# Kernel optimization log

Hardware: AMD Instinct MI355X
Metric: run time of the kernel (lower is better)

## Reference

```python
import jax, jax.numpy as jnp
import numpy as np

# Static problem sizes (must be static for segment ops under jit)
N = 2048   # num nodes (seq_len)
M = 50     # num hyperedges (hyper_num); original uses max(edge_id)+1, guaranteed hit with 8192 draws
C = 64     # out_channels (= in_channels here)
BT = 64    # batch
E = 8192   # incidences = k(=4) hyperedges per node
NEG_SLOPE = 0.2
MARGIN = 4.2


def setup_inputs() -> dict:
    key = jax.random.key(0)
    k1, k2, k3, k4, k5 = jax.random.split(key, 5)
    x = jax.random.normal(k1, (BT, N, C), jnp.float32)
    weight = jax.random.normal(k2, (C, C), jnp.float32) * (1.0 / np.sqrt(C))  # glorot-ish
    att = jax.random.normal(k3, (1, 1, 2 * C), jnp.float32) * 0.1
    node_idx = jax.random.randint(k4, (E,), 0, N, dtype=jnp.int32)
    edge_idx = jax.random.randint(k5, (E,), 0, M, dtype=jnp.int32)
    return {"x": x, "weight": weight, "att": att, "node_idx": node_idx, "edge_idx": edge_idx}


def _safe_norm(v, axis):
    # norm with zero (not NaN/inf) gradient at 0, matching torch.norm subgradient
    sq = jnp.sum(v * v, axis=axis)
    pos = sq > 0
    return jnp.where(pos, jnp.sqrt(jnp.where(pos, sq, 1.0)), 0.0)


def _segment_softmax(logits, seg, num_segments):
    # grouped softmax over incidences sharing the same node id (PyG softmax)
    mx = jax.ops.segment_max(logits, seg, num_segments=num_segments)
    mx = jnp.where(jnp.isfinite(mx), mx, 0.0)  # empty segments
    e = jnp.exp(logits - mx[seg])
    s = jax.ops.segment_sum(e, seg, num_segments=num_segments)
    return e / (s[seg] + 1e-16)


def reference(x, weight, att, node_idx, edge_idx):
    xw = jnp.einsum('bnc,cd->bnd', x, weight)          # [B,N,C] dense GEMM
    x1 = jnp.transpose(xw, (1, 0, 2))                  # [N,B,C]
    x_i = x1[node_idx]                                 # [E,B,C] gather per incidence
    edge_sums = jax.ops.segment_sum(x_i, edge_idx, num_segments=M)  # [M,B,C] per-edge aggregate
    x_j = edge_sums[edge_idx]                          # [E,B,C]

    # pairwise hyperedge contrastive loss (vectorized double loop over edges)
    inner = jnp.einsum('kbc,mbc->kmb', edge_sums, edge_sums)  # [M,M,B]
    nrm = _safe_norm(edge_sums, axis=-1)               # [M,B]
    cos = inner / (nrm[:, None, :] * nrm[None, :, :])
    diff = edge_sums[:, None] - edge_sums[None, :]     # [M,M,B,C]
    dist = _safe_norm(diff, axis=-1)                   # [M,M,B]
    loss_item = cos * dist + (1.0 - cos) * jnp.maximum(MARGIN - dist, 0.0)
    loss_hyper = jnp.sum(jnp.abs(jnp.mean(loss_item, axis=-1))) / float((M + 1) ** 2)

    # per-incidence attention, softmax grouped by node
    logits = jnp.sum(jnp.concatenate([x_i, x_j], axis=-1) * att.reshape(1, 1, 2 * C), axis=-1)  # [E,B]
    logits = jax.nn.leaky_relu(logits, NEG_SLOPE)
    alpha = _segment_softmax(logits, node_idx, N)      # [E,B] (dropout skipped: eval mode)

    ones = jnp.ones((E,), xw.dtype)
    D = jax.ops.segment_sum(ones, node_idx, num_segments=N)    # node degree
    Bdeg = jax.ops.segment_sum(ones, edge_idx, num_segments=M) # hyperedge degree
    Bnorm = jnp.where(Bdeg > 0, 1.0 / Bdeg, 0.0)

    # propagate pass 1: nodes -> hyperedges (source_to_target)
    msg1 = Bnorm[edge_idx][:, None, None] * alpha[:, :, None] * x_i
    edge_feat = jax.ops.segment_sum(msg1, edge_idx, num_segments=M)  # [M,B,C]
    # propagate pass 2: hyperedges -> nodes (target_to_source)
    msg2 = D[node_idx][:, None, None] * alpha[:, :, None] * edge_feat[edge_idx]
    out = jax.ops.segment_sum(msg2, node_idx, num_segments=N)        # [N,B,C]
    out = jnp.transpose(out, (1, 0, 2))               # [B,N,C]

    constrain_losstotal = jnp.abs(jnp.mean(x_i - x_j)) + loss_hyper
    return out, constrain_losstotal
```

## Files before the change

kernel.cpp:

```cpp
#include <hip/hip_runtime.h>
#include <math.h>

#define NN 2048
#define MM 50
#define CC 64
#define BB 64
#define EE 8192
#define NEG 0.2f
#define MARGIN_ 4.2f
#define ETILE 320
#define NPAIRBLK 625

__global__ __launch_bounds__(256) void k_build(const int* __restrict__ nidx,const int* __restrict__ eidx,
                        int* __restrict__ ncnt,int* __restrict__ noff,
                        int* __restrict__ ecnt,int* __restrict__ eoff,
                        int* __restrict__ nlist,int* __restrict__ elist){
  int t=threadIdx.x, wv=t>>6, lane=t&63;
  int seg = blockIdx.x*4 + wv;
  if (seg >= NN+MM) return;
  const int* key; int target; int* outl;
  if (seg < NN){ key=nidx; target=seg;    outl=nlist; }
  else         { key=eidx; target=seg-NN; outl=elist; }
  int base = 0;
  for (int e=lane; e<EE; e+=64) base += (key[e] < target);
  #pragma unroll
  for (int m=32;m>=1;m>>=1) base += __shfl_xor(base,m,64);
  unsigned long long ltmask = (1ull<<lane) - 1ull;
  int carry = 0;
  for (int wq=0; wq<EE/64; ++wq){
    int e = wq*64 + lane;
    bool mm = (key[e]==target);
    unsigned long long bal = __ballot(mm);
    if (mm) outl[base + carry + __popcll(bal & ltmask)] = e;
    carry += __popcll(bal);
  }
  if (lane==0){
    if (seg<NN){ ncnt[seg]=carry; noff[seg]=base; }
    else       { ecnt[seg-NN]=carry; eoff[seg-NN]=base; }
  }
}

__global__ __launch_bounds__(256) void k_gemm(const float* __restrict__ x,const float* __restrict__ w,
       const float* __restrict__ att, float* __restrict__ outf,
       float* __restrict__ natt1,float* __restrict__ natt2,
       const int* __restrict__ ncnt, float* __restrict__ gpart2){
  __shared__ float Xl[64*68];
  __shared__ float Wl[64*64];
  __shared__ float red[16];
  int t = threadIdx.x;
  size_t rbase = (size_t)blockIdx.x*64;
  {
    const float4* xs = (const float4*)(x + rbase*CC);
    const float4* wsrc = (const float4*)w;
    #pragma unroll
    for (int i=0;i<4;++i){
      int idx = t + i*256;
      int r = idx>>4, c4 = idx&15;
      float4 v = xs[idx];
      *(float4*)&Xl[r*68 + c4*4] = v;
      ((float4*)Wl)[idx] = wsrc[idx];
    }
  }
  __syncthreads();
  int rg = t>>4, cg = t&15;
  int c0 = cg*4;
  float acc[4][4];
  #pragma unroll
  for (int i=0;i<4;++i){ acc[i][0]=0.f; acc[i][1]=0.f; acc[i][2]=0.f; acc[i][3]=0.f; }
  #pragma unroll
  for (int ks=0; ks<16; ++ks){
    int k0 = ks*4;
    float4 Wf0 = *(const float4*)&Wl[(k0+0)*64 + c0];
    float4 Wf1 = *(const float4*)&Wl[(k0+1)*64 + c0];
    float4 Wf2 = *(const float4*)&Wl[(k0+2)*64 + c0];
    float4 Wf3 = *(const float4*)&Wl[(k0+3)*64 + c0];
    #pragma unroll
    for (int ri=0;ri<4;++ri){
      float4 Xf = *(const float4*)&Xl[(rg*4+ri)*68 + k0];
      acc[ri][0] += Xf.x*Wf0.x; acc[ri][1] += Xf.x*Wf0.y; acc[ri][2] += Xf.x*Wf0.z; acc[ri][3] += Xf.x*Wf0.w;
      acc[ri][0] += Xf.y*Wf1.x; acc[ri][1] += Xf.y*Wf1.y; acc[ri][2] += Xf.y*Wf1.z; acc[ri][3] += Xf.y*Wf1.w;
      acc[ri][0] += Xf.z*Wf2.x; acc[ri][1] += Xf.z*Wf2.y; acc[ri][2] += Xf.z*Wf2.z; acc[ri][3] += Xf.z*Wf2.w;
      acc[ri][0] += Xf.w*Wf3.x; acc[ri][1] += Xf.w*Wf3.y; acc[ri][2] += Xf.w*Wf3.z; acc[ri][3] += Xf.w*Wf3.w;
    }
  }
  #pragma unroll
  for (int ri=0;ri<4;++ri){
    size_t row = rbase + rg*4 + ri;
    *(float4*)&outf[row*CC + c0] = make_float4(acc[ri][0],acc[ri][1],acc[ri][2],acc[ri][3]);
  }
  float4 at1 = *(const float4*)(att + c0);
  float4 at2 = *(const float4*)(att + CC + c0);
  float prs = 0.f;
  #pragma unroll
  for (int ri=0;ri<4;++ri){
    float a1 = acc[ri][0]*at1.x + acc[ri][1]*at1.y + acc[ri][2]*at1.z + acc[ri][3]*at1.w;
    float a2 = acc[ri][0]*at2.x + acc[ri][1]*at2.y + acc[ri][2]*at2.z + acc[ri][3]*at2.w;
    float rs = (acc[ri][0]+acc[ri][1]) + (acc[ri][2]+acc[ri][3]);
    #pragma unroll
    for (int m=8;m>=1;m>>=1){
      a1 += __shfl_xor(a1,m,64);
      a2 += __shfl_xor(a2,m,64);
      rs += __shfl_xor(rs,m,64);
    }
    if (cg==0){
      size_t row = rbase + rg*4 + ri;
      int b = (int)(row>>11), n = (int)(row&(NN-1));
      natt1[n*BB+b]=a1; natt2[n*BB+b]=a2;
      prs += rs*(float)ncnt[n];
    }
  }
  if (cg==0) red[rg] = prs;
  __syncthreads();
  if (t==0){
    float s=0.f;
    #pragma unroll
    for (int i=0;i<16;++i) s += red[i];
    gpart2[blockIdx.x] = s;
  }
}

__global__ __launch_bounds__(256) void k_eatt(const int* __restrict__ elist,const int* __restrict__ eoff,
                       const int* __restrict__ ecnt,const int* __restrict__ nidx,
                       const float* __restrict__ natt2,float* __restrict__ eatt2){
  __shared__ int lds_n[ETILE];
  __shared__ float part[256];
  int m=blockIdx.x, t=threadIdx.x;
  int b = t&63, ck = t>>6;
  int off=eoff[m], deg=ecnt[m];
  float s=0.f;
  for (int tb=0; tb<deg; tb+=ETILE){
    int tl = min(ETILE, deg-tb);
    __syncthreads();
    for (int j=t;j<tl;j+=256) lds_n[j]=nidx[elist[off+tb+j]];
    __syncthreads();
    int j0=(tl*ck)>>2, j1=(tl*(ck+1))>>2;
    for (int j=j0;j<j1;++j) s += natt2[lds_n[j]*BB+b];
  }
  part[t]=s; __syncthreads();
  if (t<64) eatt2[m*BB+b] = (part[b]+part[64+b])+(part[128+b]+part[192+b]);
}

__global__ void k_alpha(const int* __restrict__ nlist,const int* __restrict__ noff,
                        const int* __restrict__ ncnt,const int* __restrict__ eidx,
                        const float* __restrict__ natt1,const float* __restrict__ eatt2,
                        float* __restrict__ alpha){
  int n = blockIdx.x, b = threadIdx.x;
  int off = noff[n], deg = ncnt[n];
  if (deg==0) return;
  float na = natt1[n*BB+b];
  float mx = -1e30f;
  for (int j=0;j<deg;++j){
    int e = nlist[off+j]; int m = eidx[e];
    float l = na + eatt2[m*BB+b]; l = l>0.f? l : NEG*l;
    mx = fmaxf(mx,l);
  }
  float s=0.f;
  for (int j=0;j<deg;++j){
    int e = nlist[off+j]; int m = eidx[e];
    float l = na + eatt2[m*BB+b]; l = l>0.f? l : NEG*l;
    s += expf(l-mx);
  }
  float inv = 1.f/(s+1e-16f);
  for (int j=0;j<deg;++j){
    int e = nlist[off+j]; int m = eidx[e];
    float l = na + eatt2[m*BB+b]; l = l>0.f? l : NEG*l;
    alpha[(size_t)e*BB+b] = expf(l-mx)*inv;
  }
}

__global__ __launch_bounds__(256) void k_edge(const int* __restrict__ elist,const int* __restrict__ eoff,
                       const int* __restrict__ ecnt,const int* __restrict__ nidx,
                       const float* __restrict__ outf,const float* __restrict__ alpha,
                       float* __restrict__ es,float* __restrict__ ef,float* __restrict__ nrm,
                       float* __restrict__ gpart3){
  __shared__ int   lds_e[ETILE];
  __shared__ int   lds_n[ETILE];
  __shared__ float lds_al[ETILE*16];
  __shared__ float red2[256];
  int m = blockIdx.x>>2, bq = blockIdx.x&3;
  int t = threadIdx.x;
  int bi = t>>4;
  int b  = bq*16 + bi;
  int c0 = (t&15)*4;
  int off = eoff[m], deg = ecnt[m];
  float4 as=make_float4(0.f,0.f,0.f,0.f), af=as;
  for (int tb=0; tb<deg; tb+=ETILE){
    int tl = min(ETILE, deg-tb);
    __syncthreads();
    for (int j=t;j<tl;j+=256){
      int e = elist[off+tb+j];
      lds_e[j]=e; lds_n[j]=nidx[e];
    }
    __syncthreads();
    for (int idx=t; idx<tl*16; idx+=256){
      int j=idx>>4, b2=idx&15;
      lds_al[idx] = alpha[(size_t)lds_e[j]*BB + bq*16 + b2];
    }
    __syncthreads();
    #pragma unroll 4
    for (int j=0;j<tl;++j){
      int n = lds_n[j];
      float al = lds_al[j*16+bi];
      float4 v = *(const float4*)&outf[(size_t)b*(NN*CC) + (size_t)n*CC + c0];
      as.x+=v.x; as.y+=v.y; as.z+=v.z; as.w+=v.w;
      af.x+=al*v.x; af.y+=al*v.y; af.z+=al*v.z; af.w+=al*v.w;
    }
  }
  float bn = deg>0 ? 1.f/(float)deg : 0.f;
  size_t o = ((size_t)m*BB+b)*CC+c0;
  *(float4*)&es[o]=as;
  float4 f; f.x=af.x*bn; f.y=af.y*bn; f.z=af.z*bn; f.w=af.w*bn;
  *(float4*)&ef[o]=f;
  float ssq = as.x*as.x+as.y*as.y+as.z*as.z+as.w*as.w;
  #pragma unroll
  for (int s=8;s>=1;s>>=1) ssq += __shfl_xor(ssq,s,64);
  if ((t&15)==0) nrm[m*BB+b] = ssq>0.f? sqrtf(ssq):0.f;
  red2[t] = (as.x+as.y)+(as.z+as.w);
  __syncthreads();
  for (int s=128;s>0;s>>=1){ if(t<s) red2[t]+=red2[t+s]; __syncthreads(); }
  if (t==0) gpart3[blockIdx.x] = red2[0]*(float)deg;
}

__global__ __launch_bounds__(256) void k_pairout(const float* __restrict__ es,const float* __restrict__ nrm,
                      float* __restrict__ pairl,
                      const int* __restrict__ nlist,const int* __restrict__ noff,
                      const int* __restrict__ ncnt,const int* __restrict__ eidx,
                      const float* __restrict__ alpha,const float* __restrict__ ef,
                      float* __restrict__ outf){
  int bid = blockIdx.x;
  int t = threadIdx.x;
  if (bid < NPAIRBLK){
    int wv = t>>6, b = t&63;
    int km = bid*4 + wv;
    if (km < MM*MM){
      int kk = km / MM, m = km % MM;
      const float4* pa = (const float4*)&es[((size_t)kk*BB+b)*CC];
      const float4* pb = (const float4*)&es[((size_t)m*BB+b)*CC];
      float inner=0.f, d2=0.f;
      #pragma unroll
      for (int q=0;q<16;++q){
        float4 a=pa[q], c=pb[q];
        inner += a.x*c.x+a.y*c.y+a.z*c.z+a.w*c.w;
        float dx=a.x-c.x, dy=a.y-c.y, dz=a.z-c.z, dw=a.w-c.w;
        d2 += dx*dx+dy*dy+dz*dz+dw*dw;
      }
      float dist = d2>0.f? sqrtf(d2):0.f;
      float cosv = inner/(nrm[kk*BB+b]*nrm[m*BB+b]);
      float li = cosv*dist + (1.f-cosv)*fmaxf(MARGIN_-dist,0.f);
      #pragma unroll
      for (int s=32;s>=1;s>>=1) li += __shfl_xor(li,s,64);
      if (b==0) pairl[km] = fabsf(li*(1.f/64.f));
    }
    return;
  }
  int n = bid - NPAIRBLK;
  int b = t>>2, sub = t&3;
  int off = noff[n], deg = ncnt[n];
  float4 a0=make_float4(0.f,0.f,0.f,0.f),a1=a0,a2=a0,a3=a0;
  for (int j=0;j<deg;++j){
    int e = nlist[off+j]; int m = eidx[e];
    float al = alpha[(size_t)e*BB+b];
    const float4* p = (const float4*)&ef[((size_t)m*BB+b)*CC + sub*16];
    float4 v0=p[0],v1=p[1],v2=p[2],v3=p[3];
    a0.x+=al*v0.x; a0.y+=al*v0.y; a0.z+=al*v0.z; a0.w+=al*v0.w;
    a1.x+=al*v1.x; a1.y+=al*v1.y; a1.z+=al*v1.z; a1.w+=al*v1.w;
    a2.x+=al*v2.x; a2.y+=al*v2.y; a2.z+=al*v2.z; a2.w+=al*v2.w;
    a3.x+=al*v3.x; a3.y+=al*v3.y; a3.z+=al*v3.z; a3.w+=al*v3.w;
  }
  float D=(float)deg;
  float* o = &outf[(size_t)b*(NN*CC) + (size_t)n*CC + sub*16];
  ((float4*)o)[0]=make_float4(D*a0.x,D*a0.y,D*a0.z,D*a0.w);
  ((float4*)o)[1]=make_float4(D*a1.x,D*a1.y,D*a1.z,D*a1.w);
  ((float4*)o)[2]=make_float4(D*a2.x,D*a2.y,D*a2.z,D*a2.w);
  ((float4*)o)[3]=make_float4(D*a3.x,D*a3.y,D*a3.z,D*a3.w);
}

__global__ void k_lfin(const float* __restrict__ pairl,const float* __restrict__ gpart2,
                       const float* __restrict__ gpart3, float* __restrict__ out){
  __shared__ float r1[256],r2[256],r3[256];
  int t=threadIdx.x;
  float s1=0.f,s2=0.f,s3=0.f;
  for (int i=t;i<MM*MM;i+=256) s1+=pairl[i];
  for (int i=t;i<(NN*BB)/64;i+=256) s2+=gpart2[i];
  for (int i=t;i<MM*4;i+=256) s3+=gpart3[i];
  r1[t]=s1;r2[t]=s2;r3[t]=s3; __syncthreads();
  for (int s=128;s>0;s>>=1){ if(t<s){r1[t]+=r1[t+s];r2[t]+=r2[t+s];r3[t]+=r3[t+s];} __syncthreads(); }
  if (t==0){
    float lh = r1[0]/2601.f;
    float con = fabsf((r2[0]-r3[0])*(1.f/33554432.f));
    out[(size_t)NN*BB*CC] = con+lh;
  }
}

extern "C" void kernel_launch(void* const* d_in, const int* in_sizes, int n_in,
                              void* d_out, int out_size, void* d_ws, size_t ws_size,
                              hipStream_t stream){
  (void)in_sizes; (void)n_in; (void)out_size; (void)ws_size;
  const float* x    = (const float*)d_in[0];
  const float* w    = (const float*)d_in[1];
  const float* att  = (const float*)d_in[2];
  const int*   nidx = (const int*)d_in[3];
  const int*   eidx = (const int*)d_in[4];
  float* outf = (float*)d_out;

  char* ws = (char*)d_ws;
  size_t off = 0;
  auto alloc = [&](size_t bytes)->void*{ void* p = ws + off; off = (off + bytes + 255) & ~(size_t)255; return p; };
  float* natt1 = (float*)alloc(sizeof(float)*NN*BB);
  float* natt2 = (float*)alloc(sizeof(float)*NN*BB);
  float* eatt2 = (float*)alloc(sizeof(float)*MM*BB);
  float* alpha = (float*)alloc(sizeof(float)*(size_t)EE*BB);
  float* es    = (float*)alloc(sizeof(float)*MM*BB*CC);
  float* ef    = (float*)alloc(sizeof(float)*MM*BB*CC);
  float* nrm   = (float*)alloc(sizeof(float)*MM*BB);
  float* pairl = (float*)alloc(sizeof(float)*MM*MM);
  float* gpart2= (float*)alloc(sizeof(float)*(NN*BB)/64);
  float* gpart3= (float*)alloc(sizeof(float)*MM*4);
  int* ncnt = (int*)alloc(sizeof(int)*NN);
  int* noff = (int*)alloc(sizeof(int)*NN);
  int* ecnt = (int*)alloc(sizeof(int)*MM);
  int* eoff = (int*)alloc(sizeof(int)*MM);
  int* nlist= (int*)alloc(sizeof(int)*EE);
  int* elist= (int*)alloc(sizeof(int)*EE);

  k_build  <<<(NN+MM+3)/4, 256, 0, stream>>>(nidx, eidx, ncnt, noff, ecnt, eoff, nlist, elist);
  k_gemm   <<<(NN*BB)/64, 256, 0, stream>>>(x, w, att, outf, natt1, natt2, ncnt, gpart2);
  k_eatt   <<<MM, 256, 0, stream>>>(elist, eoff, ecnt, nidx, natt2, eatt2);
  k_alpha  <<<NN, 64, 0, stream>>>(nlist, noff, ncnt, eidx, natt1, eatt2, alpha);
  k_edge   <<<MM*4, 256, 0, stream>>>(elist, eoff, ecnt, nidx, outf, alpha, es, ef, nrm, gpart3);
  k_pairout<<<NPAIRBLK + NN, 256, 0, stream>>>(es, nrm, pairl, nlist, noff, ncnt, eidx, alpha, ef, outf);
  k_lfin   <<<1, 256, 0, stream>>>(pairl, gpart2, gpart3, outf);
}
```

Baseline: 139.6 us.

## Merge index build with GEMM and reorganize kernel schedule into five launches

Runs the CSR index build and the x·W GEMM as one launch, with the build done by the first block range. The edge-attention term is now computed from the per-edge sums (att2 dotted with the summed features), which drops the natt2 buffer and the separate k_eatt pass. The edge-sum and norm work moves into an earlier kernel that also reduces the degree-weighted row sums. The pairwise loss now shares a launch with the softmax, and the final scalar reduction runs as an extra block of the output kernel. This cuts the launch count from seven to five and removes some scattered gathers. In exchange, the outf feature rows are read twice, once in k_es and again in k_ef, and the rowsum buffer costs an extra write and read.

```diff
diff --git a/kernel.cpp b/kernel.cpp
--- a/kernel.cpp
+++ b/kernel.cpp
@@ -10,45 +10,47 @@
 #define MARGIN_ 4.2f
 #define ETILE 320
 #define NPAIRBLK 625
-
-__global__ __launch_bounds__(256) void k_build(const int* __restrict__ nidx,const int* __restrict__ eidx,
-                        int* __restrict__ ncnt,int* __restrict__ noff,
-                        int* __restrict__ ecnt,int* __restrict__ eoff,
-                        int* __restrict__ nlist,int* __restrict__ elist){
-  int t=threadIdx.x, wv=t>>6, lane=t&63;
-  int seg = blockIdx.x*4 + wv;
-  if (seg >= NN+MM) return;
-  const int* key; int target; int* outl;
-  if (seg < NN){ key=nidx; target=seg;    outl=nlist; }
-  else         { key=eidx; target=seg-NN; outl=elist; }
-  int base = 0;
-  for (int e=lane; e<EE; e+=64) base += (key[e] < target);
-  #pragma unroll
-  for (int m=32;m>=1;m>>=1) base += __shfl_xor(base,m,64);
-  unsigned long long ltmask = (1ull<<lane) - 1ull;
-  int carry = 0;
-  for (int wq=0; wq<EE/64; ++wq){
-    int e = wq*64 + lane;
-    bool mm = (key[e]==target);
-    unsigned long long bal = __ballot(mm);
-    if (mm) outl[base + carry + __popcll(bal & ltmask)] = e;
-    carry += __popcll(bal);
-  }
-  if (lane==0){
-    if (seg<NN){ ncnt[seg]=carry; noff[seg]=base; }
-    else       { ecnt[seg-NN]=carry; eoff[seg-NN]=base; }
-  }
-}
-
-__global__ __launch_bounds__(256) void k_gemm(const float* __restrict__ x,const float* __restrict__ w,
-       const float* __restrict__ att, float* __restrict__ outf,
-       float* __restrict__ natt1,float* __restrict__ natt2,
-       const int* __restrict__ ncnt, float* __restrict__ gpart2){
+#define NBUILD 525
+
+__global__ __launch_bounds__(256) void k_bg(
+    const float* __restrict__ x, const float* __restrict__ w, const float* __restrict__ att,
+    const int* __restrict__ nidx, const int* __restrict__ eidx,
+    float* __restrict__ outf, float* __restrict__ natt1, float* __restrict__ rsBN,
+    int* __restrict__ ncnt, int* __restrict__ noff, int* __restrict__ ecnt,
+    int* __restrict__ eoff, int* __restrict__ nlist, int* __restrict__ elist){
   __shared__ float Xl[64*68];
   __shared__ float Wl[64*64];
-  __shared__ float red[16];
   int t = threadIdx.x;
-  size_t rbase = (size_t)blockIdx.x*64;
+  int bid = blockIdx.x;
+
+  if (bid < NBUILD){
+    int wv=t>>6, lane=t&63;
+    int seg = bid*4 + wv;
+    if (seg >= NN+MM) return;
+    const int* key; int target; int* outl;
+    if (seg < NN){ key=nidx; target=seg;    outl=nlist; }
+    else         { key=eidx; target=seg-NN; outl=elist; }
+    int base = 0;
+    for (int e=lane; e<EE; e+=64) base += (key[e] < target);
+    #pragma unroll
+    for (int m=32;m>=1;m>>=1) base += __shfl_xor(base,m,64);
+    unsigned long long ltmask = (1ull<<lane) - 1ull;
+    int carry = 0;
+    for (int wq=0; wq<EE/64; ++wq){
+      int e = wq*64 + lane;
+      bool mm = (key[e]==target);
+      unsigned long long bal = __ballot(mm);
+      if (mm) outl[base + carry + __popcll(bal & ltmask)] = e;
+      carry += __popcll(bal);
+    }
+    if (lane==0){
+      if (seg<NN){ ncnt[seg]=carry; noff[seg]=base; }
+      else       { ecnt[seg-NN]=carry; eoff[seg-NN]=base; }
+    }
+    return;
+  }
+
+  size_t rbase = (size_t)(bid - NBUILD)*64;
   {
     const float4* xs = (const float4*)(x + rbase*CC);
     const float4* wsrc = (const float4*)w;
@@ -89,62 +91,115 @@
     *(float4*)&outf[row*CC + c0] = make_float4(acc[ri][0],acc[ri][1],acc[ri][2],acc[ri][3]);
   }
   float4 at1 = *(const float4*)(att + c0);
-  float4 at2 = *(const float4*)(att + CC + c0);
-  float prs = 0.f;
   #pragma unroll
   for (int ri=0;ri<4;++ri){
     float a1 = acc[ri][0]*at1.x + acc[ri][1]*at1.y + acc[ri][2]*at1.z + acc[ri][3]*at1.w;
-    float a2 = acc[ri][0]*at2.x + acc[ri][1]*at2.y + acc[ri][2]*at2.z + acc[ri][3]*at2.w;
     float rs = (acc[ri][0]+acc[ri][1]) + (acc[ri][2]+acc[ri][3]);
     #pragma unroll
     for (int m=8;m>=1;m>>=1){
       a1 += __shfl_xor(a1,m,64);
-      a2 += __shfl_xor(a2,m,64);
       rs += __shfl_xor(rs,m,64);
     }
     if (cg==0){
       size_t row = rbase + rg*4 + ri;
       int b = (int)(row>>11), n = (int)(row&(NN-1));
-      natt1[n*BB+b]=a1; natt2[n*BB+b]=a2;
-      prs += rs*(float)ncnt[n];
-    }
-  }
-  if (cg==0) red[rg] = prs;
-  __syncthreads();
-  if (t==0){
-    float s=0.f;
-    #pragma unroll
-    for (int i=0;i<16;++i) s += red[i];
-    gpart2[blockIdx.x] = s;
-  }
-}
-
-__global__ __launch_bounds__(256) void k_eatt(const int* __restrict__ elist,const int* __restrict__ eoff,
-                       const int* __restrict__ ecnt,const int* __restrict__ nidx,
-                       const float* __restrict__ natt2,float* __restrict__ eatt2){
+      natt1[n*BB+b]=a1; rsBN[row]=rs;
+    }
+  }
+}
+
+__global__ __launch_bounds__(256) void k_es(
+    const int* __restrict__ elist,const int* __restrict__ eoff,
+    const int* __restrict__ ecnt,const int* __restrict__ nidx,
+    const float* __restrict__ outf,const float* __restrict__ att,
+    float* __restrict__ es,float* __restrict__ nrm,float* __restrict__ eatt2,
+    float* __restrict__ gpart3,
+    const float* __restrict__ rsBN,const int* __restrict__ ncnt,
+    float* __restrict__ gpart2){
   __shared__ int lds_n[ETILE];
-  __shared__ float part[256];
-  int m=blockIdx.x, t=threadIdx.x;
-  int b = t&63, ck = t>>6;
-  int off=eoff[m], deg=ecnt[m];
-  float s=0.f;
+  __shared__ float red2[256];
+  int bid = blockIdx.x, t = threadIdx.x;
+
+  if (bid >= MM*4){
+    int k = bid - MM*4;
+    float s = 0.f;
+    for (int i=k*256+t; i<NN*BB; i+=32*256) s += rsBN[i]*(float)ncnt[i&(NN-1)];
+    red2[t]=s; __syncthreads();
+    for (int st=128;st>0;st>>=1){ if(t<st) red2[t]+=red2[t+st]; __syncthreads(); }
+    if (t==0) gpart2[k]=red2[0];
+    return;
+  }
+
+  int m = bid>>2, bq = bid&3;
+  int bi = t>>4;
+  int b  = bq*16 + bi;
+  int c0 = (t&15)*4;
+  int off = eoff[m], deg = ecnt[m];
+  float4 as=make_float4(0.f,0.f,0.f,0.f);
   for (int tb=0; tb<deg; tb+=ETILE){
     int tl = min(ETILE, deg-tb);
     __syncthreads();
     for (int j=t;j<tl;j+=256) lds_n[j]=nidx[elist[off+tb+j]];
     __syncthreads();
-    int j0=(tl*ck)>>2, j1=(tl*(ck+1))>>2;
-    for (int j=j0;j<j1;++j) s += natt2[lds_n[j]*BB+b];
-  }
-  part[t]=s; __syncthreads();
-  if (t<64) eatt2[m*BB+b] = (part[b]+part[64+b])+(part[128+b]+part[192+b]);
-}
-
-__global__ void k_alpha(const int* __restrict__ nlist,const int* __restrict__ noff,
-                        const int* __restrict__ ncnt,const int* __restrict__ eidx,
-                        const float* __restrict__ natt1,const float* __restrict__ eatt2,
-                        float* __restrict__ alpha){
-  int n = blockIdx.x, b = threadIdx.x;
+    #pragma unroll 4
+    for (int j=0;j<tl;++j){
+      int n = lds_n[j];
+      float4 v = *(const float4*)&outf[(size_t)b*(NN*CC) + (size_t)n*CC + c0];
+      as.x+=v.x; as.y+=v.y; as.z+=v.z; as.w+=v.w;
+    }
+  }
+  size_t o = ((size_t)m*BB+b)*CC+c0;
+  *(float4*)&es[o]=as;
+  float ssq = as.x*as.x+as.y*as.y+as.z*as.z+as.w*as.w;
+  float4 at2 = *(const float4*)(att + CC + c0);
+  float ea = as.x*at2.x+as.y*at2.y+as.z*at2.z+as.w*at2.w;
+  #pragma unroll
+  for (int s=8;s>=1;s>>=1){ ssq += __shfl_xor(ssq,s,64); ea += __shfl_xor(ea,s,64); }
+  if ((t&15)==0){
+    nrm[m*BB+b] = ssq>0.f? sqrtf(ssq):0.f;
+    eatt2[m*BB+b] = ea;
+  }
+  red2[t] = (as.x+as.y)+(as.z+as.w);
+  __syncthreads();
+  for (int s=128;s>0;s>>=1){ if(t<s) red2[t]+=red2[t+s]; __syncthreads(); }
+  if (t==0) gpart3[bid] = red2[0]*(float)deg;
+}
+
+__global__ __launch_bounds__(256) void k_ap(
+    const float* __restrict__ es,const float* __restrict__ nrm,
+    float* __restrict__ pairl,
+    const int* __restrict__ nlist,const int* __restrict__ noff,
+    const int* __restrict__ ncnt,const int* __restrict__ eidx,
+    const float* __restrict__ natt1,const float* __restrict__ eatt2,
+    float* __restrict__ alpha){
+  int bid = blockIdx.x, t = threadIdx.x;
+  int wv = t>>6, b = t&63;
+
+  if (bid < NPAIRBLK){
+    int km = bid*4 + wv;
+    if (km >= MM*MM) return;
+    int kk = km / MM, m = km % MM;
+    const float4* pa = (const float4*)&es[((size_t)kk*BB+b)*CC];
+    const float4* pb = (const float4*)&es[((size_t)m*BB+b)*CC];
+    float inner=0.f, d2=0.f;
+    #pragma unroll
+    for (int q=0;q<16;++q){
+      float4 a=pa[q], c=pb[q];
+      inner += a.x*c.x+a.y*c.y+a.z*c.z+a.w*c.w;
+      float dx=a.x-c.x, dy=a.y-c.y, dz=a.z-c.z, dw=a.w-c.w;
+      d2 += dx*dx+dy*dy+dz*dz+dw*dw;
+    }
+    float dist = d2>0.f? sqrtf(d2):0.f;
+    float cosv = inner/(nrm[kk*BB+b]*nrm[m*BB+b]);
+    float li = cosv*dist + (1.f-cosv)*fmaxf(MARGIN_-dist,0.f);
+    #pragma unroll
+    for (int s=32;s>=1;s>>=1) li += __shfl_xor(li,s,64);
+    if (b==0) pairl[km] = fabsf(li*(1.f/64.f));
+    return;
+  }
+
+  int n = (bid - NPAIRBLK)*4 + wv;
+  if (n >= NN) return;
   int off = noff[n], deg = ncnt[n];
   if (deg==0) return;
   float na = natt1[n*BB+b];
@@ -168,22 +223,21 @@
   }
 }
 
-__global__ __launch_bounds__(256) void k_edge(const int* __restrict__ elist,const int* __restrict__ eoff,
-                       const int* __restrict__ ecnt,const int* __restrict__ nidx,
-                       const float* __restrict__ outf,const float* __restrict__ alpha,
-                       float* __restrict__ es,float* __restrict__ ef,float* __restrict__ nrm,
-                       float* __restrict__ gpart3){
+__global__ __launch_bounds__(256) void k_ef(
+    const int* __restrict__ elist,const int* __restrict__ eoff,
+    const int* __restrict__ ecnt,const int* __restrict__ nidx,
+    const float* __restrict__ outf,const float* __restrict__ alpha,
+    float* __restrict__ ef){
   __shared__ int   lds_e[ETILE];
   __shared__ int   lds_n[ETILE];
   __shared__ float lds_al[ETILE*16];
-  __shared__ float red2[256];
   int m = blockIdx.x>>2, bq = blockIdx.x&3;
   int t = threadIdx.x;
   int bi = t>>4;
   int b  = bq*16 + bi;
   int c0 = (t&15)*4;
   int off = eoff[m], deg = ecnt[m];
-  float4 as=make_float4(0.f,0.f,0.f,0.f), af=as;
+  float4 af=make_float4(0.f,0.f,0.f,0.f);
   for (int tb=0; tb<deg; tb+=ETILE){
     int tl = min(ETILE, deg-tb);
     __syncthreads();
@@ -202,58 +256,41 @@
       int n = lds_n[j];
       float al = lds_al[j*16+bi];
       float4 v = *(const float4*)&outf[(size_t)b*(NN*CC) + (size_t)n*CC + c0];
-      as.x+=v.x; as.y+=v.y; as.z+=v.z; as.w+=v.w;
       af.x+=al*v.x; af.y+=al*v.y; af.z+=al*v.z; af.w+=al*v.w;
     }
   }
   float bn = deg>0 ? 1.f/(float)deg : 0.f;
   size_t o = ((size_t)m*BB+b)*CC+c0;
-  *(float4*)&es[o]=as;
   float4 f; f.x=af.x*bn; f.y=af.y*bn; f.z=af.z*bn; f.w=af.w*bn;
   *(float4*)&ef[o]=f;
-  float ssq = as.x*as.x+as.y*as.y+as.z*as.z+as.w*as.w;
-  #pragma unroll
-  for (int s=8;s>=1;s>>=1) ssq += __shfl_xor(ssq,s,64);
-  if ((t&15)==0) nrm[m*BB+b] = ssq>0.f? sqrtf(ssq):0.f;
-  red2[t] = (as.x+as.y)+(as.z+as.w);
-  __syncthreads();
-  for (int s=128;s>0;s>>=1){ if(t<s) red2[t]+=red2[t+s]; __syncthreads(); }
-  if (t==0) gpart3[blockIdx.x] = red2[0]*(float)deg;
-}
-
-__global__ __launch_bounds__(256) void k_pairout(const float* __restrict__ es,const float* __restrict__ nrm,
-                      float* __restrict__ pairl,
-                      const int* __restrict__ nlist,const int* __restrict__ noff,
-                      const int* __restrict__ ncnt,const int* __restrict__ eidx,
-                      const float* __restrict__ alpha,const float* __restrict__ ef,
-                      float* __restrict__ outf){
-  int bid = blockIdx.x;
-  int t = threadIdx.x;
-  if (bid < NPAIRBLK){
-    int wv = t>>6, b = t&63;
-    int km = bid*4 + wv;
-    if (km < MM*MM){
-      int kk = km / MM, m = km % MM;
-      const float4* pa = (const float4*)&es[((size_t)kk*BB+b)*CC];
-      const float4* pb = (const float4*)&es[((size_t)m*BB+b)*CC];
-      float inner=0.f, d2=0.f;
-      #pragma unroll
-      for (int q=0;q<16;++q){
-        float4 a=pa[q], c=pb[q];
-        inner += a.x*c.x+a.y*c.y+a.z*c.z+a.w*c.w;
-        float dx=a.x-c.x, dy=a.y-c.y, dz=a.z-c.z, dw=a.w-c.w;
-        d2 += dx*dx+dy*dy+dz*dz+dw*dw;
-      }
-      float dist = d2>0.f? sqrtf(d2):0.f;
-      float cosv = inner/(nrm[kk*BB+b]*nrm[m*BB+b]);
-      float li = cosv*dist + (1.f-cosv)*fmaxf(MARGIN_-dist,0.f);
-      #pragma unroll
-      for (int s=32;s>=1;s>>=1) li += __shfl_xor(li,s,64);
-      if (b==0) pairl[km] = fabsf(li*(1.f/64.f));
+}
+
+__global__ __launch_bounds__(256) void k_outl(
+    const int* __restrict__ nlist,const int* __restrict__ noff,
+    const int* __restrict__ ncnt,const int* __restrict__ eidx,
+    const float* __restrict__ alpha,const float* __restrict__ ef,
+    const float* __restrict__ pairl,const float* __restrict__ gpart2,
+    const float* __restrict__ gpart3,
+    float* __restrict__ outf){
+  __shared__ float r1[256],r2[256],r3[256];
+  int bid = blockIdx.x, t = threadIdx.x;
+
+  if (bid == NN){
+    float s1=0.f,s2=0.f,s3=0.f;
+    for (int i=t;i<MM*MM;i+=256) s1+=pairl[i];
+    if (t<32) s2=gpart2[t];
+    for (int i=t;i<MM*4;i+=256) s3+=gpart3[i];
+    r1[t]=s1;r2[t]=s2;r3[t]=s3; __syncthreads();
+    for (int s=128;s>0;s>>=1){ if(t<s){r1[t]+=r1[t+s];r2[t]+=r2[t+s];r3[t]+=r3[t+s];} __syncthreads(); }
+    if (t==0){
+      float lh = r1[0]/2601.f;
+      float con = fabsf((r2[0]-r3[0])*(1.f/33554432.f));
+      outf[(size_t)NN*BB*CC] = con+lh;
     }
     return;
   }
-  int n = bid - NPAIRBLK;
+
+  int n = bid;
   int b = t>>2, sub = t&3;
   int off = noff[n], deg = ncnt[n];
   float4 a0=make_float4(0.f,0.f,0.f,0.f),a1=a0,a2=a0,a3=a0;
@@ -275,23 +312,6 @@
   ((float4*)o)[3]=make_float4(D*a3.x,D*a3.y,D*a3.z,D*a3.w);
 }
 
-__global__ void k_lfin(const float* __restrict__ pairl,const float* __restrict__ gpart2,
-                       const float* __restrict__ gpart3, float* __restrict__ out){
-  __shared__ float r1[256],r2[256],r3[256];
-  int t=threadIdx.x;
-  float s1=0.f,s2=0.f,s3=0.f;
-  for (int i=t;i<MM*MM;i+=256) s1+=pairl[i];
-  for (int i=t;i<(NN*BB)/64;i+=256) s2+=gpart2[i];
-  for (int i=t;i<MM*4;i+=256) s3+=gpart3[i];
-  r1[t]=s1;r2[t]=s2;r3[t]=s3; __syncthreads();
-  for (int s=128;s>0;s>>=1){ if(t<s){r1[t]+=r1[t+s];r2[t]+=r2[t+s];r3[t]+=r3[t+s];} __syncthreads(); }
-  if (t==0){
-    float lh = r1[0]/2601.f;
-    float con = fabsf((r2[0]-r3[0])*(1.f/33554432.f));
-    out[(size_t)NN*BB*CC] = con+lh;
-  }
-}
-
 extern "C" void kernel_launch(void* const* d_in, const int* in_sizes, int n_in,
                               void* d_out, int out_size, void* d_ws, size_t ws_size,
                               hipStream_t stream){
@@ -307,14 +327,14 @@
   size_t off = 0;
   auto alloc = [&](size_t bytes)->void*{ void* p = ws + off; off = (off + bytes + 255) & ~(size_t)255; return p; };
   float* natt1 = (float*)alloc(sizeof(float)*NN*BB);
-  float* natt2 = (float*)alloc(sizeof(float)*NN*BB);
   float* eatt2 = (float*)alloc(sizeof(float)*MM*BB);
   float* alpha = (float*)alloc(sizeof(float)*(size_t)EE*BB);
   float* es    = (float*)alloc(sizeof(float)*MM*BB*CC);
   float* ef    = (float*)alloc(sizeof(float)*MM*BB*CC);
   float* nrm   = (float*)alloc(sizeof(float)*MM*BB);
   float* pairl = (float*)alloc(sizeof(float)*MM*MM);
-  float* gpart2= (float*)alloc(sizeof(float)*(NN*BB)/64);
+  float* rsBN  = (float*)alloc(sizeof(float)*NN*BB);
+  float* gpart2= (float*)alloc(sizeof(float)*32);
   float* gpart3= (float*)alloc(sizeof(float)*MM*4);
   int* ncnt = (int*)alloc(sizeof(int)*NN);
   int* noff = (int*)alloc(sizeof(int)*NN);
@@ -323,11 +343,14 @@
   int* nlist= (int*)alloc(sizeof(int)*EE);
   int* elist= (int*)alloc(sizeof(int)*EE);
 
-  k_build  <<<(NN+MM+3)/4, 256, 0, stream>>>(nidx, eidx, ncnt, noff, ecnt, eoff, nlist, elist);
-  k_gemm   <<<(NN*BB)/64, 256, 0, stream>>>(x, w, att, outf, natt1, natt2, ncnt, gpart2);
-  k_eatt   <<<MM, 256, 0, stream>>>(elist, eoff, ecnt, nidx, natt2, eatt2);
-  k_alpha  <<<NN, 64, 0, stream>>>(nlist, noff, ncnt, eidx, natt1, eatt2, alpha);
-  k_edge   <<<MM*4, 256, 0, stream>>>(elist, eoff, ecnt, nidx, outf, alpha, es, ef, nrm, gpart3);
-  k_pairout<<<NPAIRBLK + NN, 256, 0, stream>>>(es, nrm, pairl, nlist, noff, ncnt, eidx, alpha, ef, outf);
-  k_lfin   <<<1, 256, 0, stream>>>(pairl, gpart2, gpart3, outf);
-}
+  k_bg  <<<NBUILD + (NN*BB)/64, 256, 0, stream>>>(x, w, att, nidx, eidx,
+                                                  outf, natt1, rsBN,
+                                                  ncnt, noff, ecnt, eoff, nlist, elist);
+  k_es  <<<MM*4 + 32, 256, 0, stream>>>(elist, eoff, ecnt, nidx, outf, att,
+                                        es, nrm, eatt2, gpart3, rsBN, ncnt, gpart2);
+  k_ap  <<<NPAIRBLK + NN/4, 256, 0, stream>>>(es, nrm, pairl,
+                                              nlist, noff, ncnt, eidx, natt1, eatt2, alpha);
+  k_ef  <<<MM*4, 256, 0, stream>>>(elist, eoff, ecnt, nidx, outf, alpha, ef);
+  k_outl<<<NN + 1, 256, 0, stream>>>(nlist, noff, ncnt, eidx, alpha, ef,
+                                     pairl, gpart2, gpart3, outf);
+}
```

New measurement: 136.4 us. 2.3% less time.
